# Optimization experiments

Measured on AMD Instinct MI355X. Metric: run time of the kernel, lower is better.

## Reference

```python
import jax, jax.numpy as jnp
import numpy as np
import math

B, T, S, C, H = 2, 2048, 2048, 1024, 16
D = C // H  # head dim = 64


def setup_inputs() -> dict:
    key = jax.random.key(0)
    ks = jax.random.split(key, 12)
    s = 1.0 / math.sqrt(C)
    inp = {
        "query": jax.random.normal(ks[0], (B, T, C), jnp.float32),
        "key": jax.random.normal(ks[1], (B, S, C), jnp.float32),
        "value": jax.random.normal(ks[2], (B, S, C), jnp.float32),
        "Wq": jax.random.normal(ks[3], (C, C), jnp.float32) * s,
        "bq": jax.random.normal(ks[4], (C,), jnp.float32) * s,
        "Wk": jax.random.normal(ks[5], (C, C), jnp.float32) * s,
        "bk": jax.random.normal(ks[6], (C,), jnp.float32) * s,
        "Wv": jax.random.normal(ks[7], (C, C), jnp.float32) * s,
        "bv": jax.random.normal(ks[8], (C,), jnp.float32) * s,
        "Wo": jax.random.normal(ks[9], (C, C), jnp.float32) * s,
        "bo": jax.random.normal(ks[10], (C,), jnp.float32) * s,
        "query_chunk_size": 1024,
    }
    return inp


def _proj_heads(x, W, b):
    # x: [B, L, C] -> [B, H, L, D]; torch nn.Linear computes x @ W.T + b
    y = x @ W.T + b
    Bv, L, _ = y.shape
    return y.reshape(Bv, L, H, D).transpose(0, 2, 1, 3)


def reference(query, key, value, Wq, bq, Wk, bk, Wv, bv, Wo, bo, query_chunk_size):
    # query_chunk_size only controls the chunked evaluation order in the
    # original; the chunked online-softmax is mathematically identical to a
    # single stable softmax, which is what we compute here.
    q = _proj_heads(query, Wq, bq) * (1.0 / math.sqrt(D))  # [B,H,T,D]
    k = _proj_heads(key, Wk, bk)                            # [B,H,S,D]
    v = _proj_heads(value, Wv, bv)                          # [B,H,S,D]
    scores = jnp.einsum('bhqd,bhkd->bhqk', q, k)            # [B,H,T,S]
    attn = jax.nn.softmax(scores, axis=-1)
    out = jnp.einsum('bhqk,bhkd->bhqd', attn, v)            # [B,H,T,D]
    out = out.transpose(0, 2, 1, 3).reshape(query.shape[0], query.shape[1], C)
    return out @ Wo.T + bo
```

## Files before the change

kernel.cpp:

```cpp
#include <hip/hip_runtime.h>
#include <math.h>


typedef __attribute__((ext_vector_type(4))) float f32x4;
typedef __attribute__((ext_vector_type(8))) __bf16 bf16x8;
typedef __attribute__((ext_vector_type(4))) unsigned int u32x4;
typedef __attribute__((ext_vector_type(2))) unsigned int u32x2;
typedef __attribute__((ext_vector_type(4))) unsigned short u16x4;

#define MFMA16(a, b, c) __builtin_amdgcn_mfma_f32_16x16x32_bf16(a, b, c, 0, 0, 0)

static __device__ __forceinline__ unsigned short f2bf(float f) {
    __bf16 h = (__bf16)f;
    return __builtin_bit_cast(unsigned short, h);
}
static __device__ __forceinline__ unsigned int pack2bf_fast(float a, float b) {
    unsigned int ua = __builtin_bit_cast(unsigned int, a) + 0x8000u;
    unsigned int ub = __builtin_bit_cast(unsigned int, b) + 0x8000u;
    return (ua >> 16) | (ub & 0xffff0000u);
}
static __device__ __forceinline__ bf16x8 cvt8(f32x4 a, f32x4 b) {
    bf16x8 t;
#pragma unroll
    for (int e = 0; e < 4; e++) { t[e] = (__bf16)a[e]; t[e + 4] = (__bf16)b[e]; }
    return t;
}

#define GLL(gptr, lptr) \
    __builtin_amdgcn_global_load_lds( \
        (const __attribute__((address_space(1))) unsigned int*)(gptr), \
        (__attribute__((address_space(3))) unsigned int*)(lptr), 16, 0, 0)

__global__ __launch_bounds__(256, 2)
void proj_qkv_kernel(const float* __restrict__ Xq, const float* __restrict__ Xk,
                     const float* __restrict__ Xv,
                     const float* __restrict__ Wq, const float* __restrict__ Wk,
                     const float* __restrict__ Wv,
                     const float* __restrict__ bq, const float* __restrict__ bk,
                     const float* __restrict__ bv,
                     unsigned short* __restrict__ qh, unsigned short* __restrict__ kh,
                     unsigned short* __restrict__ vt)
{
    const int z = blockIdx.z;
    const float* X    = (z == 0) ? Xq : (z == 1) ? Xk : Xv;
    const float* W    = (z == 0) ? Wq : (z == 1) ? Wk : Wv;
    const float* bias = (z == 0) ? bq : (z == 1) ? bk : bv;
    unsigned short* O = (z == 0) ? qh : (z == 1) ? kh : vt;
    const float scale = (z == 0) ? 0.18033688011112042f : 1.0f;

    __shared__ float Af[128 * 32];
    __shared__ float Bf[128 * 32];

    const int tid  = threadIdx.x;
    const int lane = tid & 63;
    const int w    = tid >> 6;
    const int l16  = lane & 15;
    const int quad = lane >> 4;
    const int wm   = (w >> 1) * 64;
    const int wn   = (w & 1) * 64;
    const int m0   = blockIdx.y * 128;
    const int n0   = blockIdx.x * 128;

    const int rhi = lane >> 3;
    const int cg  = (lane & 7) ^ rhi;

    f32x4 acc[4][4];
#pragma unroll
    for (int i = 0; i < 4; i++)
#pragma unroll
        for (int j = 0; j < 4; j++) {
            f32x4 zv = {0.0f, 0.0f, 0.0f, 0.0f};
            acc[i][j] = zv;
        }

    const int sA = (2 * quad) ^ (l16 & 7);

    for (int k0 = 0; k0 < 1024; k0 += 32) {
#pragma unroll
        for (int r = 0; r < 4; r++) {
            int j = w * 4 + r;
            GLL(X + (size_t)(m0 + j * 8 + rhi) * 1024 + k0 + cg * 4,
                &Af[j * 8 * 32]);
            GLL(W + (size_t)(n0 + j * 8 + rhi) * 1024 + k0 + cg * 4,
                &Bf[j * 8 * 32]);
        }
        __syncthreads();

        bf16x8 af[4], bfr[4];
#pragma unroll
        for (int mi = 0; mi < 4; mi++) {
            const float* p = &Af[(wm + mi * 16 + l16) * 32];
            f32x4 c0 = *(const f32x4*)(p + sA * 4);
            f32x4 c1 = *(const f32x4*)(p + (sA ^ 1) * 4);
            af[mi] = cvt8(c0, c1);
        }
#pragma unroll
        for (int ni = 0; ni < 4; ni++) {
            const float* p = &Bf[(wn + ni * 16 + l16) * 32];
            f32x4 c0 = *(const f32x4*)(p + sA * 4);
            f32x4 c1 = *(const f32x4*)(p + (sA ^ 1) * 4);
            bfr[ni] = cvt8(c0, c1);
        }
        if (z != 2) {
#pragma unroll
            for (int mi = 0; mi < 4; mi++)
#pragma unroll
                for (int ni = 0; ni < 4; ni++)
                    acc[mi][ni] = MFMA16(af[mi], bfr[ni], acc[mi][ni]);
        } else {
#pragma unroll
            for (int mi = 0; mi < 4; mi++)
#pragma unroll
                for (int ni = 0; ni < 4; ni++)
                    acc[mi][ni] = MFMA16(bfr[ni], af[mi], acc[mi][ni]);
        }
        __syncthreads();
    }

    if (z != 2) {
#pragma unroll
        for (int ni = 0; ni < 4; ni++) {
            int gn = n0 + wn + ni * 16 + l16;
            float bval = bias[gn];
            int h = gn >> 6, d = gn & 63;
#pragma unroll
            for (int mi = 0; mi < 4; mi++) {
#pragma unroll
                for (int r = 0; r < 4; r++) {
                    int gm = m0 + wm + mi * 16 + quad * 4 + r;
                    int b = gm >> 11, l = gm & 2047;
                    float val = (acc[mi][ni][r] + bval) * scale;
                    O[(((size_t)(b * 16 + h) * 2048 + l) * 64) + d] = f2bf(val);
                }
            }
        }
    } else {
#pragma unroll
        for (int ni = 0; ni < 4; ni++) {
#pragma unroll
            for (int r = 0; r < 4; r++) {
                int gn = n0 + wn + ni * 16 + quad * 4 + r;
                float bval = bias[gn];
                int h = gn >> 6, d = gn & 63;
#pragma unroll
                for (int mi = 0; mi < 4; mi++) {
                    int gm = m0 + wm + mi * 16 + l16;
                    int b = gm >> 11, l = gm & 2047;
                    O[((size_t)(b * 16 + h) * 64 + d) * 2048 + l] =
                        f2bf(acc[mi][ni][r] + bval);
                }
            }
        }
    }
}

__global__ __launch_bounds__(256, 2)
void attn_kernel(const unsigned short* __restrict__ qh,
                 const unsigned short* __restrict__ kh,
                 const unsigned short* __restrict__ vt,
                 unsigned short* __restrict__ ao)
{
    __shared__ unsigned short Kl[2][64 * 64];
    __shared__ unsigned short Vl[2][64 * 64];
    __shared__ unsigned short Ps[8 * 1024];

    const int tid  = threadIdx.x;
    const int lane = tid & 63;
    const int w    = tid >> 6;
    const int l16  = lane & 15;
    const int quad = lane >> 4;
    const int qt   = blockIdx.x;
    const int bh   = blockIdx.y;

    const unsigned short* Qb = qh + (size_t)bh * 2048 * 64;
    const unsigned short* Kb = kh + (size_t)bh * 2048 * 64;
    const unsigned short* Vb = vt + (size_t)bh * 64 * 2048;

    const int qbase = qt * 128 + w * 32;

    const int rhi = lane >> 3;
    const int cg  = (lane & 7) ^ rhi;

    auto stage = [&](int s0t, int buf) {
#pragma unroll
        for (int r = 0; r < 2; r++) {
            int j = w * 2 + r;
            GLL(Kb + (size_t)(s0t + j * 8 + rhi) * 64 + cg * 8, &Kl[buf][j * 512]);
            GLL(Vb + (size_t)(j * 8 + rhi) * 2048 + s0t + cg * 8, &Vl[buf][j * 512]);
        }
    };

    bf16x8 qf[2][2];
#pragma unroll
    for (int qg = 0; qg < 2; qg++)
#pragma unroll
        for (int ks = 0; ks < 2; ks++)
            qf[qg][ks] = *(const bf16x8*)(Qb +
                (size_t)(qbase + qg * 16 + l16) * 64 + ks * 32 + quad * 8);

    f32x4 oacc[2][4];
#pragma unroll
    for (int qg = 0; qg < 2; qg++)
#pragma unroll
        for (int di = 0; di < 4; di++) {
            f32x4 zv = {0.0f, 0.0f, 0.0f, 0.0f};
            oacc[qg][di] = zv;
        }
    float l_[2] = {0.0f, 0.0f};

    unsigned short* Pw0 = Ps + (w * 2 + 0) * 1024;
    unsigned short* Pw1 = Ps + (w * 2 + 1) * 1024;

    const int c0 = (quad ^ (l16 & 7)) * 8;
    const int c1 = c0 ^ 32;

    stage(0, 0);
    __syncthreads();

    int buf = 0;
    for (int s0 = 0; s0 < 2048; s0 += 64) {
        if (s0 + 64 < 2048) stage(s0 + 64, buf ^ 1);

        const unsigned short* Kc = &Kl[buf][0];
        const unsigned short* Vc = &Vl[buf][0];

        bf16x8 kf[4][2], vf[4][2];
#pragma unroll
        for (int si = 0; si < 4; si++) {
            const unsigned short* kp = Kc + (si * 16 + l16) * 64;
            kf[si][0] = *(const bf16x8*)(kp + c0);
            kf[si][1] = *(const bf16x8*)(kp + c1);
        }
#pragma unroll
        for (int di = 0; di < 4; di++) {
            const unsigned short* vp = Vc + (di * 16 + l16) * 64;
            vf[di][0] = *(const bf16x8*)(vp + c0);
            vf[di][1] = *(const bf16x8*)(vp + c1);
        }

        f32x4 sacc[2][4];
#pragma unroll
        for (int qg = 0; qg < 2; qg++)
#pragma unroll
            for (int si = 0; si < 4; si++) {
                f32x4 sv = {-16.0f, -16.0f, -16.0f, -16.0f};
                sacc[qg][si] = sv;
            }
#pragma unroll
        for (int si = 0; si < 4; si++) {
            sacc[0][si] = MFMA16(kf[si][0], qf[0][0], sacc[0][si]);
            sacc[1][si] = MFMA16(kf[si][0], qf[1][0], sacc[1][si]);
            sacc[0][si] = MFMA16(kf[si][1], qf[0][1], sacc[0][si]);
            sacc[1][si] = MFMA16(kf[si][1], qf[1][1], sacc[1][si]);
        }

#pragma unroll
        for (int qg = 0; qg < 2; qg++) {
            float sum = 0.0f;
#pragma unroll
            for (int si = 0; si < 4; si++)
#pragma unroll
                for (int r = 0; r < 4; r++) {
                    float p = exp2f(sacc[qg][si][r]);
                    sacc[qg][si][r] = p;
                    sum += p;
                }
            l_[qg] += sum;
        }

#pragma unroll
        for (int si = 0; si < 4; si++) {
            int sc    = si >> 1;
            int quadp = (si & 1) * 2 + (quad >> 1);
            int off   = (sc * 64 + quadp * 16 + l16) * 8 + (quad & 1) * 4;
            u32x2 dw0, dw1;
            dw0[0] = pack2bf_fast(sacc[0][si][0], sacc[0][si][1]);
            dw0[1] = pack2bf_fast(sacc[0][si][2], sacc[0][si][3]);
            dw1[0] = pack2bf_fast(sacc[1][si][0], sacc[1][si][1]);
            dw1[1] = pack2bf_fast(sacc[1][si][2], sacc[1][si][3]);
            *(u32x2*)(Pw0 + off) = dw0;
            *(u32x2*)(Pw1 + off) = dw1;
        }

#pragma unroll
        for (int sc = 0; sc < 2; sc++) {
            bf16x8 pf0 = *(const bf16x8*)(Pw0 + (sc * 64 + lane) * 8);
            bf16x8 pf1 = *(const bf16x8*)(Pw1 + (sc * 64 + lane) * 8);
#pragma unroll
            for (int di = 0; di < 4; di++) {
                oacc[0][di] = MFMA16(vf[di][sc], pf0, oacc[0][di]);
                oacc[1][di] = MFMA16(vf[di][sc], pf1, oacc[1][di]);
            }
        }

        __syncthreads();
        buf ^= 1;
    }

    const int b = bh >> 4, h = bh & 15;
#pragma unroll
    for (int qg = 0; qg < 2; qg++) {
        float lt = l_[qg];
        lt += __shfl_xor(lt, 16, 64);
        lt += __shfl_xor(lt, 32, 64);
        float inv = 1.0f / lt;
        int q16 = qbase + qg * 16 + l16;
#pragma unroll
        for (int di = 0; di < 4; di++) {
            u16x4 pk;
#pragma unroll
            for (int r = 0; r < 4; r++) pk[r] = f2bf(oacc[qg][di][r] * inv);
            *(u16x4*)(ao + (size_t)(b * 2048 + q16) * 1024 +
                      h * 64 + di * 16 + quad * 4) = pk;
        }
    }
}

__global__ __launch_bounds__(256, 2)
void proj_out_kernel(const unsigned short* __restrict__ A,
                     const float* __restrict__ W,
                     const float* __restrict__ bias,
                     float* __restrict__ out)
{
    __shared__ unsigned short As[128 * 32];
    __shared__ float Bf[128 * 32];

    const int tid  = threadIdx.x;
    const int lane = tid & 63;
    const int w    = tid >> 6;
    const int l16  = lane & 15;
    const int quad = lane >> 4;
    const int wm   = (w >> 1) * 64;
    const int wn   = (w & 1) * 64;
    const int m0   = blockIdx.y * 128;
    const int n0   = blockIdx.x * 128;

    const int rhiA = lane >> 2;
    const int cgA  = (lane & 3) ^ (rhiA & 3);
    const int rhiB = lane >> 3;
    const int cgB  = (lane & 7) ^ rhiB;

    f32x4 acc[4][4];
#pragma unroll
    for (int i = 0; i < 4; i++)
#pragma unroll
        for (int j = 0; j < 4; j++) {
            f32x4 zv = {0.0f, 0.0f, 0.0f, 0.0f};
            acc[i][j] = zv;
        }

    const int sB = (2 * quad) ^ (l16 & 7);
    const int sAq = quad ^ (l16 & 3);

    for (int k0 = 0; k0 < 1024; k0 += 32) {
#pragma unroll
        for (int r = 0; r < 2; r++) {
            int j = w * 2 + r;
            GLL(A + (size_t)(m0 + j * 16 + rhiA) * 1024 + k0 + cgA * 8,
                &As[j * 16 * 32]);
        }
#pragma unroll
        for (int r = 0; r < 4; r++) {
            int j = w * 4 + r;
            GLL(W + (size_t)(n0 + j * 8 + rhiB) * 1024 + k0 + cgB * 4,
                &Bf[j * 8 * 32]);
        }
        __syncthreads();

        bf16x8 af[4], bfr[4];
#pragma unroll
        for (int mi = 0; mi < 4; mi++)
            af[mi] = *(const bf16x8*)(&As[(wm + mi * 16 + l16) * 32 + sAq * 8]);
#pragma unroll
        for (int ni = 0; ni < 4; ni++) {
            const float* p = &Bf[(wn + ni * 16 + l16) * 32];
            f32x4 cb0 = *(const f32x4*)(p + sB * 4);
            f32x4 cb1 = *(const f32x4*)(p + (sB ^ 1) * 4);
            bfr[ni] = cvt8(cb0, cb1);
        }
#pragma unroll
        for (int mi = 0; mi < 4; mi++)
#pragma unroll
            for (int ni = 0; ni < 4; ni++)
                acc[mi][ni] = MFMA16(af[mi], bfr[ni], acc[mi][ni]);
        __syncthreads();
    }

#pragma unroll
    for (int ni = 0; ni < 4; ni++) {
        int gn = n0 + wn + ni * 16 + l16;
        float bval = bias[gn];
#pragma unroll
        for (int mi = 0; mi < 4; mi++) {
#pragma unroll
            for (int r = 0; r < 4; r++) {
                int gm = m0 + wm + mi * 16 + quad * 4 + r;
                out[(size_t)gm * 1024 + gn] = acc[mi][ni][r] + bval;
            }
        }
    }
}

extern "C" void kernel_launch(void* const* d_in, const int* in_sizes, int n_in,
                              void* d_out, int out_size, void* d_ws, size_t ws_size,
                              hipStream_t stream)
{
    const float* query = (const float*)d_in[0];
    const float* key   = (const float*)d_in[1];
    const float* value = (const float*)d_in[2];
    const float* Wq    = (const float*)d_in[3];
    const float* bq    = (const float*)d_in[4];
    const float* Wk    = (const float*)d_in[5];
    const float* bk    = (const float*)d_in[6];
    const float* Wv    = (const float*)d_in[7];
    const float* bv    = (const float*)d_in[8];
    const float* Wo    = (const float*)d_in[9];
    const float* bo    = (const float*)d_in[10];

    unsigned short* qh = (unsigned short*)d_ws;
    unsigned short* kh = qh + 4194304;
    unsigned short* vt = kh + 4194304;
    unsigned short* ao = vt + 4194304;
    float* out = (float*)d_out;

    proj_qkv_kernel<<<dim3(8, 32, 3), 256, 0, stream>>>(
        query, key, value, Wq, Wk, Wv, bq, bk, bv, qh, kh, vt);
    attn_kernel<<<dim3(16, 32), 256, 0, stream>>>(qh, kh, vt, ao);
    proj_out_kernel<<<dim3(8, 32), 256, 0, stream>>>(ao, Wo, bo, out);
}
```

Baseline: 299.3 us.

## Pre-convert inputs and weights to bf16 before the projection GEMMs

Adds a conversion kernel that turns the fp32 activations and all four weight matrices into bf16 in workspace. New bf16 projection kernels then stage half-size tiles through LDS and feed MFMA directly, with no per-iteration fp32-to-bf16 conversion. The output projection also uses 64-row tiles to launch more blocks. This costs an extra pass over the fp32 inputs and needs a larger workspace, so it is guarded by a workspace-size check and falls back to the old path otherwise.

```diff
diff --git a/kernel.cpp b/kernel.cpp
--- a/kernel.cpp
+++ b/kernel.cpp
@@ -30,6 +30,381 @@
     __builtin_amdgcn_global_load_lds( \
         (const __attribute__((address_space(1))) unsigned int*)(gptr), \
         (__attribute__((address_space(3))) unsigned int*)(lptr), 16, 0, 0)
+
+__global__ __launch_bounds__(256)
+void cvt_kernel(const float* __restrict__ xq, const float* __restrict__ xk,
+                const float* __restrict__ xv,
+                const float* __restrict__ wq, const float* __restrict__ wk,
+                const float* __restrict__ wv, const float* __restrict__ wo,
+                unsigned short* __restrict__ xbf, unsigned short* __restrict__ wbf)
+{
+    const int t = blockIdx.y;
+    const float* src;
+    unsigned short* dst;
+    int n;
+    if (t < 3) {
+        src = (t == 0) ? xq : (t == 1) ? xk : xv;
+        dst = xbf + (size_t)t * 4194304;
+        n = 4194304;
+    } else {
+        int u = t - 3;
+        src = (u == 0) ? wq : (u == 1) ? wk : (u == 2) ? wv : wo;
+        dst = wbf + (size_t)u * 1048576;
+        n = 1048576;
+    }
+    for (int i = (blockIdx.x * 256 + threadIdx.x) * 4; i < n; i += gridDim.x * 1024) {
+        f32x4 x = *(const f32x4*)(src + i);
+        u16x4 h;
+#pragma unroll
+        for (int e = 0; e < 4; e++) h[e] = f2bf(x[e]);
+        *(u16x4*)(dst + i) = h;
+    }
+}
+
+__global__ __launch_bounds__(256, 3)
+void proj_qkv_bf16_kernel(const unsigned short* __restrict__ xbf,
+                          const unsigned short* __restrict__ wbf,
+                          const float* __restrict__ bq, const float* __restrict__ bk,
+                          const float* __restrict__ bv,
+                          unsigned short* __restrict__ qh, unsigned short* __restrict__ kh,
+                          unsigned short* __restrict__ vt)
+{
+    const int z = blockIdx.z;
+    const unsigned short* X = xbf + (size_t)z * 4194304;
+    const unsigned short* W = wbf + (size_t)z * 1048576;
+    const float* bias = (z == 0) ? bq : (z == 1) ? bk : bv;
+    unsigned short* O = (z == 0) ? qh : (z == 1) ? kh : vt;
+    const float scale = (z == 0) ? 0.18033688011112042f : 1.0f;
+
+    __shared__ unsigned short As[128 * 32];
+    __shared__ unsigned short Bs[128 * 32];
+
+    const int tid  = threadIdx.x;
+    const int lane = tid & 63;
+    const int w    = tid >> 6;
+    const int l16  = lane & 15;
+    const int quad = lane >> 4;
+    const int wm   = (w >> 1) * 64;
+    const int wn   = (w & 1) * 64;
+    const int m0   = blockIdx.y * 128;
+    const int n0   = blockIdx.x * 128;
+
+    const int rhi = lane >> 2;
+    const int cg  = (lane & 3) ^ (rhi & 3);
+
+    f32x4 acc[4][4];
+#pragma unroll
+    for (int i = 0; i < 4; i++)
+#pragma unroll
+        for (int j = 0; j < 4; j++) {
+            f32x4 zv = {0.0f, 0.0f, 0.0f, 0.0f};
+            acc[i][j] = zv;
+        }
+
+    const int sl = (quad ^ (l16 & 3)) * 8;
+
+    for (int k0 = 0; k0 < 1024; k0 += 32) {
+#pragma unroll
+        for (int r = 0; r < 2; r++) {
+            int j = w * 2 + r;
+            GLL(X + (size_t)(m0 + j * 16 + rhi) * 1024 + k0 + cg * 8, &As[j * 512]);
+            GLL(W + (size_t)(n0 + j * 16 + rhi) * 1024 + k0 + cg * 8, &Bs[j * 512]);
+        }
+        __syncthreads();
+
+        bf16x8 af[4], bfr[4];
+#pragma unroll
+        for (int mi = 0; mi < 4; mi++)
+            af[mi] = *(const bf16x8*)(&As[(wm + mi * 16 + l16) * 32 + sl]);
+#pragma unroll
+        for (int ni = 0; ni < 4; ni++)
+            bfr[ni] = *(const bf16x8*)(&Bs[(wn + ni * 16 + l16) * 32 + sl]);
+        if (z != 2) {
+#pragma unroll
+            for (int mi = 0; mi < 4; mi++)
+#pragma unroll
+                for (int ni = 0; ni < 4; ni++)
+                    acc[mi][ni] = MFMA16(af[mi], bfr[ni], acc[mi][ni]);
+        } else {
+#pragma unroll
+            for (int mi = 0; mi < 4; mi++)
+#pragma unroll
+                for (int ni = 0; ni < 4; ni++)
+                    acc[mi][ni] = MFMA16(bfr[ni], af[mi], acc[mi][ni]);
+        }
+        __syncthreads();
+    }
+
+    if (z != 2) {
+#pragma unroll
+        for (int ni = 0; ni < 4; ni++) {
+            int gn = n0 + wn + ni * 16 + l16;
+            float bval = bias[gn];
+            int h = gn >> 6, d = gn & 63;
+#pragma unroll
+            for (int mi = 0; mi < 4; mi++) {
+#pragma unroll
+                for (int r = 0; r < 4; r++) {
+                    int gm = m0 + wm + mi * 16 + quad * 4 + r;
+                    int b = gm >> 11, l = gm & 2047;
+                    float val = (acc[mi][ni][r] + bval) * scale;
+                    O[(((size_t)(b * 16 + h) * 2048 + l) * 64) + d] = f2bf(val);
+                }
+            }
+        }
+    } else {
+#pragma unroll
+        for (int ni = 0; ni < 4; ni++) {
+#pragma unroll
+            for (int r = 0; r < 4; r++) {
+                int gn = n0 + wn + ni * 16 + quad * 4 + r;
+                float bval = bias[gn];
+                int h = gn >> 6, d = gn & 63;
+#pragma unroll
+                for (int mi = 0; mi < 4; mi++) {
+                    int gm = m0 + wm + mi * 16 + l16;
+                    int b = gm >> 11, l = gm & 2047;
+                    O[((size_t)(b * 16 + h) * 64 + d) * 2048 + l] =
+                        f2bf(acc[mi][ni][r] + bval);
+                }
+            }
+        }
+    }
+}
+
+__global__ __launch_bounds__(256, 2)
+void attn_kernel(const unsigned short* __restrict__ qh,
+                 const unsigned short* __restrict__ kh,
+                 const unsigned short* __restrict__ vt,
+                 unsigned short* __restrict__ ao)
+{
+    __shared__ unsigned short Kl[2][64 * 64];
+    __shared__ unsigned short Vl[2][64 * 64];
+    __shared__ unsigned short Ps[8 * 1024];
+
+    const int tid  = threadIdx.x;
+    const int lane = tid & 63;
+    const int w    = tid >> 6;
+    const int l16  = lane & 15;
+    const int quad = lane >> 4;
+    const int qt   = blockIdx.x;
+    const int bh   = blockIdx.y;
+
+    const unsigned short* Qb = qh + (size_t)bh * 2048 * 64;
+    const unsigned short* Kb = kh + (size_t)bh * 2048 * 64;
+    const unsigned short* Vb = vt + (size_t)bh * 64 * 2048;
+
+    const int qbase = qt * 128 + w * 32;
+
+    const int rhi = lane >> 3;
+    const int cg  = (lane & 7) ^ rhi;
+
+    auto stage = [&](int s0t, int buf) {
+#pragma unroll
+        for (int r = 0; r < 2; r++) {
+            int j = w * 2 + r;
+            GLL(Kb + (size_t)(s0t + j * 8 + rhi) * 64 + cg * 8, &Kl[buf][j * 512]);
+            GLL(Vb + (size_t)(j * 8 + rhi) * 2048 + s0t + cg * 8, &Vl[buf][j * 512]);
+        }
+    };
+
+    bf16x8 qf[2][2];
+#pragma unroll
+    for (int qg = 0; qg < 2; qg++)
+#pragma unroll
+        for (int ks = 0; ks < 2; ks++)
+            qf[qg][ks] = *(const bf16x8*)(Qb +
+                (size_t)(qbase + qg * 16 + l16) * 64 + ks * 32 + quad * 8);
+
+    f32x4 oacc[2][4];
+#pragma unroll
+    for (int qg = 0; qg < 2; qg++)
+#pragma unroll
+        for (int di = 0; di < 4; di++) {
+            f32x4 zv = {0.0f, 0.0f, 0.0f, 0.0f};
+            oacc[qg][di] = zv;
+        }
+    float l_[2] = {0.0f, 0.0f};
+
+    unsigned short* Pw0 = Ps + (w * 2 + 0) * 1024;
+    unsigned short* Pw1 = Ps + (w * 2 + 1) * 1024;
+
+    const int c0 = (quad ^ (l16 & 7)) * 8;
+    const int c1 = c0 ^ 32;
+
+    stage(0, 0);
+    __syncthreads();
+
+    int buf = 0;
+    for (int s0 = 0; s0 < 2048; s0 += 64) {
+        if (s0 + 64 < 2048) stage(s0 + 64, buf ^ 1);
+
+        const unsigned short* Kc = &Kl[buf][0];
+        const unsigned short* Vc = &Vl[buf][0];
+
+        bf16x8 kf[4][2], vf[4][2];
+#pragma unroll
+        for (int si = 0; si < 4; si++) {
+            const unsigned short* kp = Kc + (si * 16 + l16) * 64;
+            kf[si][0] = *(const bf16x8*)(kp + c0);
+            kf[si][1] = *(const bf16x8*)(kp + c1);
+        }
+#pragma unroll
+        for (int di = 0; di < 4; di++) {
+            const unsigned short* vp = Vc + (di * 16 + l16) * 64;
+            vf[di][0] = *(const bf16x8*)(vp + c0);
+            vf[di][1] = *(const bf16x8*)(vp + c1);
+        }
+
+        f32x4 sacc[2][4];
+#pragma unroll
+        for (int qg = 0; qg < 2; qg++)
+#pragma unroll
+            for (int si = 0; si < 4; si++) {
+                f32x4 sv = {-16.0f, -16.0f, -16.0f, -16.0f};
+                sacc[qg][si] = sv;
+            }
+#pragma unroll
+        for (int si = 0; si < 4; si++) {
+            sacc[0][si] = MFMA16(kf[si][0], qf[0][0], sacc[0][si]);
+            sacc[1][si] = MFMA16(kf[si][0], qf[1][0], sacc[1][si]);
+            sacc[0][si] = MFMA16(kf[si][1], qf[0][1], sacc[0][si]);
+            sacc[1][si] = MFMA16(kf[si][1], qf[1][1], sacc[1][si]);
+        }
+
+#pragma unroll
+        for (int qg = 0; qg < 2; qg++) {
+            float sum = 0.0f;
+#pragma unroll
+            for (int si = 0; si < 4; si++)
+#pragma unroll
+                for (int r = 0; r < 4; r++) {
+                    float p = exp2f(sacc[qg][si][r]);
+                    sacc[qg][si][r] = p;
+                    sum += p;
+                }
+            l_[qg] += sum;
+        }
+
+#pragma unroll
+        for (int si = 0; si < 4; si++) {
+            int sc    = si >> 1;
+            int quadp = (si & 1) * 2 + (quad >> 1);
+            int off   = (sc * 64 + quadp * 16 + l16) * 8 + (quad & 1) * 4;
+            u32x2 dw0, dw1;
+            dw0[0] = pack2bf_fast(sacc[0][si][0], sacc[0][si][1]);
+            dw0[1] = pack2bf_fast(sacc[0][si][2], sacc[0][si][3]);
+            dw1[0] = pack2bf_fast(sacc[1][si][0], sacc[1][si][1]);
+            dw1[1] = pack2bf_fast(sacc[1][si][2], sacc[1][si][3]);
+            *(u32x2*)(Pw0 + off) = dw0;
+            *(u32x2*)(Pw1 + off) = dw1;
+        }
+
+#pragma unroll
+        for (int sc = 0; sc < 2; sc++) {
+            bf16x8 pf0 = *(const bf16x8*)(Pw0 + (sc * 64 + lane) * 8);
+            bf16x8 pf1 = *(const bf16x8*)(Pw1 + (sc * 64 + lane) * 8);
+#pragma unroll
+            for (int di = 0; di < 4; di++) {
+                oacc[0][di] = MFMA16(vf[di][sc], pf0, oacc[0][di]);
+                oacc[1][di] = MFMA16(vf[di][sc], pf1, oacc[1][di]);
+            }
+        }
+
+        __syncthreads();
+        buf ^= 1;
+    }
+
+    const int b = bh >> 4, h = bh & 15;
+#pragma unroll
+    for (int qg = 0; qg < 2; qg++) {
+        float lt = l_[qg];
+        lt += __shfl_xor(lt, 16, 64);
+        lt += __shfl_xor(lt, 32, 64);
+        float inv = 1.0f / lt;
+        int q16 = qbase + qg * 16 + l16;
+#pragma unroll
+        for (int di = 0; di < 4; di++) {
+            u16x4 pk;
+#pragma unroll
+            for (int r = 0; r < 4; r++) pk[r] = f2bf(oacc[qg][di][r] * inv);
+            *(u16x4*)(ao + (size_t)(b * 2048 + q16) * 1024 +
+                      h * 64 + di * 16 + quad * 4) = pk;
+        }
+    }
+}
+
+__global__ __launch_bounds__(256, 4)
+void proj_out_bf16_kernel(const unsigned short* __restrict__ A,
+                          const unsigned short* __restrict__ Wb,
+                          const float* __restrict__ bias,
+                          float* __restrict__ out)
+{
+    __shared__ unsigned short As[64 * 32];
+    __shared__ unsigned short Bs[128 * 32];
+
+    const int tid  = threadIdx.x;
+    const int lane = tid & 63;
+    const int w    = tid >> 6;
+    const int l16  = lane & 15;
+    const int quad = lane >> 4;
+    const int wm   = (w >> 1) * 32;
+    const int wn   = (w & 1) * 64;
+    const int m0   = blockIdx.y * 64;
+    const int n0   = blockIdx.x * 128;
+
+    const int rhi = lane >> 2;
+    const int cg  = (lane & 3) ^ (rhi & 3);
+
+    f32x4 acc[2][4];
+#pragma unroll
+    for (int i = 0; i < 2; i++)
+#pragma unroll
+        for (int j = 0; j < 4; j++) {
+            f32x4 zv = {0.0f, 0.0f, 0.0f, 0.0f};
+            acc[i][j] = zv;
+        }
+
+    const int sl = (quad ^ (l16 & 3)) * 8;
+
+    for (int k0 = 0; k0 < 1024; k0 += 32) {
+        GLL(A + (size_t)(m0 + w * 16 + rhi) * 1024 + k0 + cg * 8, &As[w * 512]);
+#pragma unroll
+        for (int r = 0; r < 2; r++) {
+            int j = w * 2 + r;
+            GLL(Wb + (size_t)(n0 + j * 16 + rhi) * 1024 + k0 + cg * 8, &Bs[j * 512]);
+        }
+        __syncthreads();
+
+        bf16x8 af[2], bfr[4];
+#pragma unroll
+        for (int mi = 0; mi < 2; mi++)
+            af[mi] = *(const bf16x8*)(&As[(wm + mi * 16 + l16) * 32 + sl]);
+#pragma unroll
+        for (int ni = 0; ni < 4; ni++)
+            bfr[ni] = *(const bf16x8*)(&Bs[(wn + ni * 16 + l16) * 32 + sl]);
+#pragma unroll
+        for (int mi = 0; mi < 2; mi++)
+#pragma unroll
+            for (int ni = 0; ni < 4; ni++)
+                acc[mi][ni] = MFMA16(af[mi], bfr[ni], acc[mi][ni]);
+        __syncthreads();
+    }
+
+#pragma unroll
+    for (int ni = 0; ni < 4; ni++) {
+        int gn = n0 + wn + ni * 16 + l16;
+        float bval = bias[gn];
+#pragma unroll
+        for (int mi = 0; mi < 2; mi++) {
+#pragma unroll
+            for (int r = 0; r < 4; r++) {
+                int gm = m0 + wm + mi * 16 + quad * 4 + r;
+                out[(size_t)gm * 1024 + gn] = acc[mi][ni][r] + bval;
+            }
+        }
+    }
+}
 
 __global__ __launch_bounds__(256, 2)
 void proj_qkv_kernel(const float* __restrict__ Xq, const float* __restrict__ Xk,
@@ -79,10 +454,8 @@
 #pragma unroll
         for (int r = 0; r < 4; r++) {
             int j = w * 4 + r;
-            GLL(X + (size_t)(m0 + j * 8 + rhi) * 1024 + k0 + cg * 4,
-                &Af[j * 8 * 32]);
-            GLL(W + (size_t)(n0 + j * 8 + rhi) * 1024 + k0 + cg * 4,
-                &Bf[j * 8 * 32]);
+            GLL(X + (size_t)(m0 + j * 8 + rhi) * 1024 + k0 + cg * 4, &Af[j * 8 * 32]);
+            GLL(W + (size_t)(n0 + j * 8 + rhi) * 1024 + k0 + cg * 4, &Bf[j * 8 * 32]);
         }
         __syncthreads();
 
@@ -90,16 +463,16 @@
 #pragma unroll
         for (int mi = 0; mi < 4; mi++) {
             const float* p = &Af[(wm + mi * 16 + l16) * 32];
-            f32x4 c0 = *(const f32x4*)(p + sA * 4);
-            f32x4 c1 = *(const f32x4*)(p + (sA ^ 1) * 4);
-            af[mi] = cvt8(c0, c1);
+            f32x4 ca = *(const f32x4*)(p + sA * 4);
+            f32x4 cb = *(const f32x4*)(p + (sA ^ 1) * 4);
+            af[mi] = cvt8(ca, cb);
         }
 #pragma unroll
         for (int ni = 0; ni < 4; ni++) {
             const float* p = &Bf[(wn + ni * 16 + l16) * 32];
-            f32x4 c0 = *(const f32x4*)(p + sA * 4);
-            f32x4 c1 = *(const f32x4*)(p + (sA ^ 1) * 4);
-            bfr[ni] = cvt8(c0, c1);
+            f32x4 ca = *(const f32x4*)(p + sA * 4);
+            f32x4 cb = *(const f32x4*)(p + (sA ^ 1) * 4);
+            bfr[ni] = cvt8(ca, cb);
         }
         if (z != 2) {
 #pragma unroll
@@ -150,168 +523,6 @@
                         f2bf(acc[mi][ni][r] + bval);
                 }
             }
-        }
-    }
-}
-
-__global__ __launch_bounds__(256, 2)
-void attn_kernel(const unsigned short* __restrict__ qh,
-                 const unsigned short* __restrict__ kh,
-                 const unsigned short* __restrict__ vt,
-                 unsigned short* __restrict__ ao)
-{
-    __shared__ unsigned short Kl[2][64 * 64];
-    __shared__ unsigned short Vl[2][64 * 64];
-    __shared__ unsigned short Ps[8 * 1024];
-
-    const int tid  = threadIdx.x;
-    const int lane = tid & 63;
-    const int w    = tid >> 6;
-    const int l16  = lane & 15;
-    const int quad = lane >> 4;
-    const int qt   = blockIdx.x;
-    const int bh   = blockIdx.y;
-
-    const unsigned short* Qb = qh + (size_t)bh * 2048 * 64;
-    const unsigned short* Kb = kh + (size_t)bh * 2048 * 64;
-    const unsigned short* Vb = vt + (size_t)bh * 64 * 2048;
-
-    const int qbase = qt * 128 + w * 32;
-
-    const int rhi = lane >> 3;
-    const int cg  = (lane & 7) ^ rhi;
-
-    auto stage = [&](int s0t, int buf) {
-#pragma unroll
-        for (int r = 0; r < 2; r++) {
-            int j = w * 2 + r;
-            GLL(Kb + (size_t)(s0t + j * 8 + rhi) * 64 + cg * 8, &Kl[buf][j * 512]);
-            GLL(Vb + (size_t)(j * 8 + rhi) * 2048 + s0t + cg * 8, &Vl[buf][j * 512]);
-        }
-    };
-
-    bf16x8 qf[2][2];
-#pragma unroll
-    for (int qg = 0; qg < 2; qg++)
-#pragma unroll
-        for (int ks = 0; ks < 2; ks++)
-            qf[qg][ks] = *(const bf16x8*)(Qb +
-                (size_t)(qbase + qg * 16 + l16) * 64 + ks * 32 + quad * 8);
-
-    f32x4 oacc[2][4];
-#pragma unroll
-    for (int qg = 0; qg < 2; qg++)
-#pragma unroll
-        for (int di = 0; di < 4; di++) {
-            f32x4 zv = {0.0f, 0.0f, 0.0f, 0.0f};
-            oacc[qg][di] = zv;
-        }
-    float l_[2] = {0.0f, 0.0f};
-
-    unsigned short* Pw0 = Ps + (w * 2 + 0) * 1024;
-    unsigned short* Pw1 = Ps + (w * 2 + 1) * 1024;
-
-    const int c0 = (quad ^ (l16 & 7)) * 8;
-    const int c1 = c0 ^ 32;
-
-    stage(0, 0);
-    __syncthreads();
-
-    int buf = 0;
-    for (int s0 = 0; s0 < 2048; s0 += 64) {
-        if (s0 + 64 < 2048) stage(s0 + 64, buf ^ 1);
-
-        const unsigned short* Kc = &Kl[buf][0];
-        const unsigned short* Vc = &Vl[buf][0];
-
-        bf16x8 kf[4][2], vf[4][2];
-#pragma unroll
-        for (int si = 0; si < 4; si++) {
-            const unsigned short* kp = Kc + (si * 16 + l16) * 64;
-            kf[si][0] = *(const bf16x8*)(kp + c0);
-            kf[si][1] = *(const bf16x8*)(kp + c1);
-        }
-#pragma unroll
-        for (int di = 0; di < 4; di++) {
-            const unsigned short* vp = Vc + (di * 16 + l16) * 64;
-            vf[di][0] = *(const bf16x8*)(vp + c0);
-            vf[di][1] = *(const bf16x8*)(vp + c1);
-        }
-
-        f32x4 sacc[2][4];
-#pragma unroll
-        for (int qg = 0; qg < 2; qg++)
-#pragma unroll
-            for (int si = 0; si < 4; si++) {
-                f32x4 sv = {-16.0f, -16.0f, -16.0f, -16.0f};
-                sacc[qg][si] = sv;
-            }
-#pragma unroll
-        for (int si = 0; si < 4; si++) {
-            sacc[0][si] = MFMA16(kf[si][0], qf[0][0], sacc[0][si]);
-            sacc[1][si] = MFMA16(kf[si][0], qf[1][0], sacc[1][si]);
-            sacc[0][si] = MFMA16(kf[si][1], qf[0][1], sacc[0][si]);
-            sacc[1][si] = MFMA16(kf[si][1], qf[1][1], sacc[1][si]);
-        }
-
-#pragma unroll
-        for (int qg = 0; qg < 2; qg++) {
-            float sum = 0.0f;
-#pragma unroll
-            for (int si = 0; si < 4; si++)
-#pragma unroll
-                for (int r = 0; r < 4; r++) {
-                    float p = exp2f(sacc[qg][si][r]);
-                    sacc[qg][si][r] = p;
-                    sum += p;
-                }
-            l_[qg] += sum;
-        }
-
-#pragma unroll
-        for (int si = 0; si < 4; si++) {
-            int sc    = si >> 1;
-            int quadp = (si & 1) * 2 + (quad >> 1);
-            int off   = (sc * 64 + quadp * 16 + l16) * 8 + (quad & 1) * 4;
-            u32x2 dw0, dw1;
-            dw0[0] = pack2bf_fast(sacc[0][si][0], sacc[0][si][1]);
-            dw0[1] = pack2bf_fast(sacc[0][si][2], sacc[0][si][3]);
-            dw1[0] = pack2bf_fast(sacc[1][si][0], sacc[1][si][1]);
-            dw1[1] = pack2bf_fast(sacc[1][si][2], sacc[1][si][3]);
-            *(u32x2*)(Pw0 + off) = dw0;
-            *(u32x2*)(Pw1 + off) = dw1;
-        }
-
-#pragma unroll
-        for (int sc = 0; sc < 2; sc++) {
-            bf16x8 pf0 = *(const bf16x8*)(Pw0 + (sc * 64 + lane) * 8);
-            bf16x8 pf1 = *(const bf16x8*)(Pw1 + (sc * 64 + lane) * 8);
-#pragma unroll
-            for (int di = 0; di < 4; di++) {
-                oacc[0][di] = MFMA16(vf[di][sc], pf0, oacc[0][di]);
-                oacc[1][di] = MFMA16(vf[di][sc], pf1, oacc[1][di]);
-            }
-        }
-
-        __syncthreads();
-        buf ^= 1;
-    }
-
-    const int b = bh >> 4, h = bh & 15;
-#pragma unroll
-    for (int qg = 0; qg < 2; qg++) {
-        float lt = l_[qg];
-        lt += __shfl_xor(lt, 16, 64);
-        lt += __shfl_xor(lt, 32, 64);
-        float inv = 1.0f / lt;
-        int q16 = qbase + qg * 16 + l16;
-#pragma unroll
-        for (int di = 0; di < 4; di++) {
-            u16x4 pk;
-#pragma unroll
-            for (int r = 0; r < 4; r++) pk[r] = f2bf(oacc[qg][di][r] * inv);
-            *(u16x4*)(ao + (size_t)(b * 2048 + q16) * 1024 +
-                      h * 64 + di * 16 + quad * 4) = pk;
         }
     }
 }
@@ -349,21 +560,19 @@
             acc[i][j] = zv;
         }
 
-    const int sB = (2 * quad) ^ (l16 & 7);
+    const int sB  = (2 * quad) ^ (l16 & 7);
     const int sAq = quad ^ (l16 & 3);
 
     for (int k0 = 0; k0 < 1024; k0 += 32) {
 #pragma unroll
         for (int r = 0; r < 2; r++) {
             int j = w * 2 + r;
-            GLL(A + (size_t)(m0 + j * 16 + rhiA) * 1024 + k0 + cgA * 8,
-                &As[j * 16 * 32]);
+            GLL(A + (size_t)(m0 + j * 16 + rhiA) * 1024 + k0 + cgA * 8, &As[j * 16 * 32]);
         }
 #pragma unroll
         for (int r = 0; r < 4; r++) {
             int j = w * 4 + r;
-            GLL(W + (size_t)(n0 + j * 8 + rhiB) * 1024 + k0 + cgB * 4,
-                &Bf[j * 8 * 32]);
+            GLL(W + (size_t)(n0 + j * 8 + rhiB) * 1024 + k0 + cgB * 4, &Bf[j * 8 * 32]);
         }
         __syncthreads();
 
@@ -423,8 +632,20 @@
     unsigned short* ao = vt + 4194304;
     float* out = (float*)d_out;
 
-    proj_qkv_kernel<<<dim3(8, 32, 3), 256, 0, stream>>>(
-        query, key, value, Wq, Wk, Wv, bq, bk, bv, qh, kh, vt);
-    attn_kernel<<<dim3(16, 32), 256, 0, stream>>>(qh, kh, vt, ao);
-    proj_out_kernel<<<dim3(8, 32), 256, 0, stream>>>(ao, Wo, bo, out);
-}
+    if (ws_size >= (size_t)64 * 1024 * 1024) {
+        unsigned short* xbf = ao + 4194304;
+        unsigned short* wbf = xbf + 12582912;
+        cvt_kernel<<<dim3(256, 7), 256, 0, stream>>>(
+            query, key, value, Wq, Wk, Wv, Wo, xbf, wbf);
+        proj_qkv_bf16_kernel<<<dim3(8, 32, 3), 256, 0, stream>>>(
+            xbf, wbf, bq, bk, bv, qh, kh, vt);
+        attn_kernel<<<dim3(16, 32), 256, 0, stream>>>(qh, kh, vt, ao);
+        proj_out_bf16_kernel<<<dim3(8, 64), 256, 0, stream>>>(
+            ao, wbf + 3 * 1048576, bo, out);
+    } else {
+        proj_qkv_kernel<<<dim3(8, 32, 3), 256, 0, stream>>>(
+            query, key, value, Wq, Wk, Wv, bq, bk, bv, qh, kh, vt);
+        attn_kernel<<<dim3(16, 32), 256, 0, stream>>>(qh, kh, vt, ao);
+        proj_out_kernel<<<dim3(8, 32), 256, 0, stream>>>(ao, Wo, bo, out);
+    }
+}
```

New measurement: 309.7 us. 1.03x slower.

## Halve attention and output-projection tiles to launch more blocks

Applied to the files above, without the earlier changes.

The attention kernel now gives each wave 16 query rows instead of 32, with each block covering 64 queries. This doubles the grid to 1024 blocks, shrinks the P staging buffer and raises the launch-bounds occupancy target to 4. The output projection moves from 128-row to 64-row M tiles, doubling its grid, and writes its results with nontemporal stores. Together these aim to fill more of the GPU's compute units, at the cost of reloading each K/V tile for twice as many blocks and doing less MFMA work per shared-memory load.

```diff
diff --git a/kernel.cpp b/kernel.cpp
--- a/kernel.cpp
+++ b/kernel.cpp
@@ -79,10 +79,8 @@
 #pragma unroll
         for (int r = 0; r < 4; r++) {
             int j = w * 4 + r;
-            GLL(X + (size_t)(m0 + j * 8 + rhi) * 1024 + k0 + cg * 4,
-                &Af[j * 8 * 32]);
-            GLL(W + (size_t)(n0 + j * 8 + rhi) * 1024 + k0 + cg * 4,
-                &Bf[j * 8 * 32]);
+            GLL(X + (size_t)(m0 + j * 8 + rhi) * 1024 + k0 + cg * 4, &Af[j * 8 * 32]);
+            GLL(W + (size_t)(n0 + j * 8 + rhi) * 1024 + k0 + cg * 4, &Bf[j * 8 * 32]);
         }
         __syncthreads();
 
@@ -90,16 +88,16 @@
 #pragma unroll
         for (int mi = 0; mi < 4; mi++) {
             const float* p = &Af[(wm + mi * 16 + l16) * 32];
-            f32x4 c0 = *(const f32x4*)(p + sA * 4);
-            f32x4 c1 = *(const f32x4*)(p + (sA ^ 1) * 4);
-            af[mi] = cvt8(c0, c1);
+            f32x4 ca = *(const f32x4*)(p + sA * 4);
+            f32x4 cb = *(const f32x4*)(p + (sA ^ 1) * 4);
+            af[mi] = cvt8(ca, cb);
         }
 #pragma unroll
         for (int ni = 0; ni < 4; ni++) {
             const float* p = &Bf[(wn + ni * 16 + l16) * 32];
-            f32x4 c0 = *(const f32x4*)(p + sA * 4);
-            f32x4 c1 = *(const f32x4*)(p + (sA ^ 1) * 4);
-            bfr[ni] = cvt8(c0, c1);
+            f32x4 ca = *(const f32x4*)(p + sA * 4);
+            f32x4 cb = *(const f32x4*)(p + (sA ^ 1) * 4);
+            bfr[ni] = cvt8(ca, cb);
         }
         if (z != 2) {
 #pragma unroll
@@ -154,7 +152,7 @@
     }
 }
 
-__global__ __launch_bounds__(256, 2)
+__global__ __launch_bounds__(256, 4)
 void attn_kernel(const unsigned short* __restrict__ qh,
                  const unsigned short* __restrict__ kh,
                  const unsigned short* __restrict__ vt,
@@ -162,7 +160,7 @@
 {
     __shared__ unsigned short Kl[2][64 * 64];
     __shared__ unsigned short Vl[2][64 * 64];
-    __shared__ unsigned short Ps[8 * 1024];
+    __shared__ unsigned short Ps[4 * 1024];
 
     const int tid  = threadIdx.x;
     const int lane = tid & 63;
@@ -176,7 +174,7 @@
     const unsigned short* Kb = kh + (size_t)bh * 2048 * 64;
     const unsigned short* Vb = vt + (size_t)bh * 64 * 2048;
 
-    const int qbase = qt * 128 + w * 32;
+    const int qbase = qt * 64 + w * 16;
 
     const int rhi = lane >> 3;
     const int cg  = (lane & 7) ^ rhi;
@@ -190,26 +188,21 @@
         }
     };
 
-    bf16x8 qf[2][2];
-#pragma unroll
-    for (int qg = 0; qg < 2; qg++)
-#pragma unroll
-        for (int ks = 0; ks < 2; ks++)
-            qf[qg][ks] = *(const bf16x8*)(Qb +
-                (size_t)(qbase + qg * 16 + l16) * 64 + ks * 32 + quad * 8);
-
-    f32x4 oacc[2][4];
-#pragma unroll
-    for (int qg = 0; qg < 2; qg++)
-#pragma unroll
-        for (int di = 0; di < 4; di++) {
-            f32x4 zv = {0.0f, 0.0f, 0.0f, 0.0f};
-            oacc[qg][di] = zv;
-        }
-    float l_[2] = {0.0f, 0.0f};
-
-    unsigned short* Pw0 = Ps + (w * 2 + 0) * 1024;
-    unsigned short* Pw1 = Ps + (w * 2 + 1) * 1024;
+    bf16x8 qf[2];
+#pragma unroll
+    for (int ks = 0; ks < 2; ks++)
+        qf[ks] = *(const bf16x8*)(Qb +
+            (size_t)(qbase + l16) * 64 + ks * 32 + quad * 8);
+
+    f32x4 oacc[4];
+#pragma unroll
+    for (int di = 0; di < 4; di++) {
+        f32x4 zv = {0.0f, 0.0f, 0.0f, 0.0f};
+        oacc[di] = zv;
+    }
+    float l_ = 0.0f;
+
+    unsigned short* Pw = Ps + w * 1024;
 
     const int c0 = (quad ^ (l16 & 7)) * 8;
     const int c1 = c0 ^ 32;
@@ -238,59 +231,46 @@
             vf[di][1] = *(const bf16x8*)(vp + c1);
         }
 
-        f32x4 sacc[2][4];
-#pragma unroll
-        for (int qg = 0; qg < 2; qg++)
-#pragma unroll
-            for (int si = 0; si < 4; si++) {
-                f32x4 sv = {-16.0f, -16.0f, -16.0f, -16.0f};
-                sacc[qg][si] = sv;
+        f32x4 sacc[4];
+#pragma unroll
+        for (int si = 0; si < 4; si++) {
+            f32x4 sv = {-16.0f, -16.0f, -16.0f, -16.0f};
+            sacc[si] = sv;
+        }
+#pragma unroll
+        for (int si = 0; si < 4; si++) {
+            sacc[si] = MFMA16(kf[si][0], qf[0], sacc[si]);
+            sacc[si] = MFMA16(kf[si][1], qf[1], sacc[si]);
+        }
+
+        float sum = 0.0f;
+#pragma unroll
+        for (int si = 0; si < 4; si++)
+#pragma unroll
+            for (int r = 0; r < 4; r++) {
+                float p = exp2f(sacc[si][r]);
+                sacc[si][r] = p;
+                sum += p;
             }
-#pragma unroll
-        for (int si = 0; si < 4; si++) {
-            sacc[0][si] = MFMA16(kf[si][0], qf[0][0], sacc[0][si]);
-            sacc[1][si] = MFMA16(kf[si][0], qf[1][0], sacc[1][si]);
-            sacc[0][si] = MFMA16(kf[si][1], qf[0][1], sacc[0][si]);
-            sacc[1][si] = MFMA16(kf[si][1], qf[1][1], sacc[1][si]);
-        }
-
-#pragma unroll
-        for (int qg = 0; qg < 2; qg++) {
-            float sum = 0.0f;
-#pragma unroll
-            for (int si = 0; si < 4; si++)
-#pragma unroll
-                for (int r = 0; r < 4; r++) {
-                    float p = exp2f(sacc[qg][si][r]);
-                    sacc[qg][si][r] = p;
-                    sum += p;
-                }
-            l_[qg] += sum;
-        }
+        l_ += sum;
 
 #pragma unroll
         for (int si = 0; si < 4; si++) {
             int sc    = si >> 1;
             int quadp = (si & 1) * 2 + (quad >> 1);
             int off   = (sc * 64 + quadp * 16 + l16) * 8 + (quad & 1) * 4;
-            u32x2 dw0, dw1;
-            dw0[0] = pack2bf_fast(sacc[0][si][0], sacc[0][si][1]);
-            dw0[1] = pack2bf_fast(sacc[0][si][2], sacc[0][si][3]);
-            dw1[0] = pack2bf_fast(sacc[1][si][0], sacc[1][si][1]);
-            dw1[1] = pack2bf_fast(sacc[1][si][2], sacc[1][si][3]);
-            *(u32x2*)(Pw0 + off) = dw0;
-            *(u32x2*)(Pw1 + off) = dw1;
+            u32x2 dw;
+            dw[0] = pack2bf_fast(sacc[si][0], sacc[si][1]);
+            dw[1] = pack2bf_fast(sacc[si][2], sacc[si][3]);
+            *(u32x2*)(Pw + off) = dw;
         }
 
 #pragma unroll
         for (int sc = 0; sc < 2; sc++) {
-            bf16x8 pf0 = *(const bf16x8*)(Pw0 + (sc * 64 + lane) * 8);
-            bf16x8 pf1 = *(const bf16x8*)(Pw1 + (sc * 64 + lane) * 8);
-#pragma unroll
-            for (int di = 0; di < 4; di++) {
-                oacc[0][di] = MFMA16(vf[di][sc], pf0, oacc[0][di]);
-                oacc[1][di] = MFMA16(vf[di][sc], pf1, oacc[1][di]);
-            }
+            bf16x8 pf = *(const bf16x8*)(Pw + (sc * 64 + lane) * 8);
+#pragma unroll
+            for (int di = 0; di < 4; di++)
+                oacc[di] = MFMA16(vf[di][sc], pf, oacc[di]);
         }
 
         __syncthreads();
@@ -298,21 +278,18 @@
     }
 
     const int b = bh >> 4, h = bh & 15;
-#pragma unroll
-    for (int qg = 0; qg < 2; qg++) {
-        float lt = l_[qg];
-        lt += __shfl_xor(lt, 16, 64);
-        lt += __shfl_xor(lt, 32, 64);
-        float inv = 1.0f / lt;
-        int q16 = qbase + qg * 16 + l16;
-#pragma unroll
-        for (int di = 0; di < 4; di++) {
-            u16x4 pk;
-#pragma unroll
-            for (int r = 0; r < 4; r++) pk[r] = f2bf(oacc[qg][di][r] * inv);
-            *(u16x4*)(ao + (size_t)(b * 2048 + q16) * 1024 +
-                      h * 64 + di * 16 + quad * 4) = pk;
-        }
+    float lt = l_;
+    lt += __shfl_xor(lt, 16, 64);
+    lt += __shfl_xor(lt, 32, 64);
+    float inv = 1.0f / lt;
+    int q16 = qbase + l16;
+#pragma unroll
+    for (int di = 0; di < 4; di++) {
+        u16x4 pk;
+#pragma unroll
+        for (int r = 0; r < 4; r++) pk[r] = f2bf(oacc[di][r] * inv);
+        *(u16x4*)(ao + (size_t)(b * 2048 + q16) * 1024 +
+                  h * 64 + di * 16 + quad * 4) = pk;
     }
 }
 
@@ -322,7 +299,7 @@
                      const float* __restrict__ bias,
                      float* __restrict__ out)
 {
-    __shared__ unsigned short As[128 * 32];
+    __shared__ unsigned short As[64 * 32];
     __shared__ float Bf[128 * 32];
 
     const int tid  = threadIdx.x;
@@ -330,9 +307,9 @@
     const int w    = tid >> 6;
     const int l16  = lane & 15;
     const int quad = lane >> 4;
-    const int wm   = (w >> 1) * 64;
+    const int wm   = (w >> 1) * 32;
     const int wn   = (w & 1) * 64;
-    const int m0   = blockIdx.y * 128;
+    const int m0   = blockIdx.y * 64;
     const int n0   = blockIdx.x * 128;
 
     const int rhiA = lane >> 2;
@@ -340,36 +317,30 @@
     const int rhiB = lane >> 3;
     const int cgB  = (lane & 7) ^ rhiB;
 
-    f32x4 acc[4][4];
-#pragma unroll
-    for (int i = 0; i < 4; i++)
+    f32x4 acc[2][4];
+#pragma unroll
+    for (int i = 0; i < 2; i++)
 #pragma unroll
         for (int j = 0; j < 4; j++) {
             f32x4 zv = {0.0f, 0.0f, 0.0f, 0.0f};
             acc[i][j] = zv;
         }
 
-    const int sB = (2 * quad) ^ (l16 & 7);
+    const int sB  = (2 * quad) ^ (l16 & 7);
     const int sAq = quad ^ (l16 & 3);
 
     for (int k0 = 0; k0 < 1024; k0 += 32) {
-#pragma unroll
-        for (int r = 0; r < 2; r++) {
-            int j = w * 2 + r;
-            GLL(A + (size_t)(m0 + j * 16 + rhiA) * 1024 + k0 + cgA * 8,
-                &As[j * 16 * 32]);
-        }
+        GLL(A + (size_t)(m0 + w * 16 + rhiA) * 1024 + k0 + cgA * 8, &As[w * 512]);
 #pragma unroll
         for (int r = 0; r < 4; r++) {
             int j = w * 4 + r;
-            GLL(W + (size_t)(n0 + j * 8 + rhiB) * 1024 + k0 + cgB * 4,
-                &Bf[j * 8 * 32]);
+            GLL(W + (size_t)(n0 + j * 8 + rhiB) * 1024 + k0 + cgB * 4, &Bf[j * 8 * 32]);
         }
         __syncthreads();
 
-        bf16x8 af[4], bfr[4];
-#pragma unroll
-        for (int mi = 0; mi < 4; mi++)
+        bf16x8 af[2], bfr[4];
+#pragma unroll
+        for (int mi = 0; mi < 2; mi++)
             af[mi] = *(const bf16x8*)(&As[(wm + mi * 16 + l16) * 32 + sAq * 8]);
 #pragma unroll
         for (int ni = 0; ni < 4; ni++) {
@@ -379,7 +350,7 @@
             bfr[ni] = cvt8(cb0, cb1);
         }
 #pragma unroll
-        for (int mi = 0; mi < 4; mi++)
+        for (int mi = 0; mi < 2; mi++)
 #pragma unroll
             for (int ni = 0; ni < 4; ni++)
                 acc[mi][ni] = MFMA16(af[mi], bfr[ni], acc[mi][ni]);
@@ -391,11 +362,12 @@
         int gn = n0 + wn + ni * 16 + l16;
         float bval = bias[gn];
 #pragma unroll
-        for (int mi = 0; mi < 4; mi++) {
+        for (int mi = 0; mi < 2; mi++) {
 #pragma unroll
             for (int r = 0; r < 4; r++) {
                 int gm = m0 + wm + mi * 16 + quad * 4 + r;
-                out[(size_t)gm * 1024 + gn] = acc[mi][ni][r] + bval;
+                __builtin_nontemporal_store(acc[mi][ni][r] + bval,
+                                            out + (size_t)gm * 1024 + gn);
             }
         }
     }
@@ -425,6 +397,6 @@
 
     proj_qkv_kernel<<<dim3(8, 32, 3), 256, 0, stream>>>(
         query, key, value, Wq, Wk, Wv, bq, bk, bv, qh, kh, vt);
-    attn_kernel<<<dim3(16, 32), 256, 0, stream>>>(qh, kh, vt, ao);
-    proj_out_kernel<<<dim3(8, 32), 256, 0, stream>>>(ao, Wo, bo, out);
-}
+    attn_kernel<<<dim3(32, 32), 256, 0, stream>>>(qh, kh, vt, ao);
+    proj_out_kernel<<<dim3(8, 64), 256, 0, stream>>>(ao, Wo, bo, out);
+}
```

After: 288.2 us. -3.7%, faster.
